# Performance work log

Hardware: AMD Instinct MI355X
Metric: run time of the kernel (lower is better)

Reference implementation:

```python
import jax, jax.numpy as jnp
import numpy as np

B, C, H, W = 32, 256, 56, 56
HEADS, M, EXP = 8, 7, 4


def _rel_pos_index(m):
    # Swin V1 pair-wise relative position index, [m*m, m*m] (static)
    coords = np.stack(np.meshgrid(np.arange(m), np.arange(m), indexing='ij'))  # [2,m,m]
    cf = coords.reshape(2, -1)
    rel = (cf[:, :, None] - cf[:, None, :]).transpose(1, 2, 0).copy()
    rel[:, :, 0] += m - 1
    rel[:, :, 1] += m - 1
    rel[:, :, 0] *= 2 * m - 1
    return jnp.asarray(rel.sum(-1))


def setup_inputs():
    key = jax.random.key(0)
    ks = jax.random.split(key, 8)
    s = lambda k, shp: jax.random.normal(k, shp, jnp.float32) * 0.02
    return {
        'x': jax.random.normal(ks[0], (B, C, H, W), jnp.float32),
        'qkv_w': s(ks[1], (3 * C, C)), 'qkv_b': jnp.zeros((3 * C,), jnp.float32),
        'proj_w': s(ks[2], (C, C)), 'proj_b': jnp.zeros((C,), jnp.float32),
        'bias_table': s(ks[3], ((2 * M - 1) * (2 * M - 1), HEADS)),
        'ln1_g': jnp.ones((C,), jnp.float32), 'ln1_b': jnp.zeros((C,), jnp.float32),
        'ln2_g': jnp.ones((C,), jnp.float32), 'ln2_b': jnp.zeros((C,), jnp.float32),
        'w1': s(ks[4], (EXP * C, C)), 'b1': jnp.zeros((EXP * C,), jnp.float32),
        'w2': s(ks[5], (C, EXP * C)), 'b2': jnp.zeros((C,), jnp.float32),
    }


def _layernorm(x, g, b, eps=1e-5):
    mu = x.mean(-1, keepdims=True)
    var = ((x - mu) ** 2).mean(-1, keepdims=True)
    return (x - mu) * jax.lax.rsqrt(var + eps) * g + b


def _block(x, qkv_w, qkv_b, proj_w, proj_b, bias_table,
           ln1_g, ln1_b, ln2_g, ln2_b, w1, b1, w2, b2):
    Bx, Cx, Hx, Wx = x.shape
    N = M * M
    # window partition: [B,C,H,W] -> [B*nw, M*M, C]
    xp = x.reshape(Bx, Cx, Hx // M, M, Wx // M, M)
    xp = xp.transpose(0, 2, 4, 3, 5, 1).reshape(-1, N, Cx)
    B_ = xp.shape[0]
    # relative self-attention (pre-LN)
    h = _layernorm(xp, ln1_g, ln1_b)
    qkv = (h @ qkv_w.T + qkv_b).reshape(B_, N, 3, HEADS, Cx // HEADS)
    qkv = qkv.transpose(2, 0, 3, 1, 4)  # [3,B_,H,N,d]
    q, k, v = qkv[0], qkv[1], qkv[2]
    q = q * (HEADS ** -0.5)  # note: module scales by num_heads**-0.5 (faithful)
    rel_idx = _rel_pos_index(M)
    bias = bias_table[rel_idx.reshape(-1)].reshape(N, N, HEADS).transpose(2, 0, 1)
    attn = jax.nn.softmax(jnp.einsum('bhnd,bhmd->bhnm', q, k) + bias[None], axis=-1)
    out = jnp.einsum('bhnm,bhmd->bhnd', attn, v).transpose(0, 2, 1, 3).reshape(B_, N, Cx)
    xp = xp + (out @ proj_w.T + proj_b)
    # MLP (1x1 Conv1d == pointwise linear), exact GELU as in torch
    h2 = _layernorm(xp, ln2_g, ln2_b)
    h2 = jax.nn.gelu(h2 @ w1.T + b1, approximate=False)
    xp = xp + (h2 @ w2.T + b2)
    # window reverse: [B*nw, M*M, C] -> [B,C,H,W]
    nwh, nww = Hx // M, Wx // M
    y = xp.reshape(Bx, nwh, nww, M, M, Cx).transpose(0, 5, 1, 3, 2, 4).reshape(Bx, Cx, Hx, Wx)
    return y


def reference(x, qkv_w, qkv_b, proj_w, proj_b, bias_table,
              ln1_g, ln1_b, ln2_g, ln2_b, w1, b1, w2, b2):
    return _block(x, qkv_w, qkv_b, proj_w, proj_b, bias_table,
                  ln1_g, ln1_b, ln2_g, ln2_b, w1, b1, w2, b2)
```

## Files before the change

### kernel.cpp

```cpp
#include <hip/hip_runtime.h>
#include <math.h>

#define TB 256

typedef short bf16x8 __attribute__((ext_vector_type(8)));
typedef short s16x4 __attribute__((ext_vector_type(4)));
typedef float f32x4 __attribute__((ext_vector_type(4)));
typedef unsigned short u16;

__device__ __forceinline__ float b2f(u16 u){
  union{unsigned i; float f;} v; v.i=((unsigned)u)<<16; return v.f;
}
__device__ __forceinline__ u16 f2b(float f){
  union{float ff; unsigned i;} v; v.ff=f;
  return (u16)((v.i + 0x7FFFu + ((v.i>>16)&1u))>>16);
}

__device__ __forceinline__ float gelu(float x){
  float z = fabsf(x)*0.70710678118654752f;
  float t = 1.0f/fmaf(0.3275911f, z, 1.0f);
  float p = t*fmaf(t, fmaf(t, fmaf(t, fmaf(t, 1.061405429f, -1.453152027f), 1.421413741f), -0.284496736f), 0.254829592f);
  float erfz = fmaf(-p, __expf(-z*z), 1.0f);
  float s = (x >= 0.f) ? erfz : -erfz;
  return 0.5f*x*(1.0f + s);
}

__global__ void k_prep(const float* __restrict__ qkv_w, const float* __restrict__ proj_w,
                       const float* __restrict__ w1, const float* __restrict__ w2,
                       const float* __restrict__ btab,
                       u16* __restrict__ wq, u16* __restrict__ wp,
                       u16* __restrict__ w1b, u16* __restrict__ w2b,
                       float* __restrict__ biasT){
  int i = blockIdx.x*TB + threadIdx.x;
  if(i < 196608){ wq[i] = f2b(qkv_w[i]); return; }
  i -= 196608;
  if(i < 65536){ wp[i] = f2b(proj_w[i]); return; }
  i -= 65536;
  if(i < 262144){ w1b[i] = f2b(w1[i]); return; }
  i -= 262144;
  if(i < 262144){ w2b[i] = f2b(w2[i]); return; }
  i -= 262144;
  if(i < 32768){
    int h = i>>12, kq = i&4095, k = kq>>6, q = kq&63;
    float v = 0.f;
    if(k<49 && q<49){
      int qi=q/7, qj=q-qi*7, ki=k/7, kj=k-ki*7;
      v = btab[((qi-ki+6)*13 + (qj-kj+6))*8 + h];
    }
    biasT[i] = v;
  }
}

__global__ __launch_bounds__(256) void k_post(const u16* __restrict__ x2lin, float* __restrict__ out){
  __shared__ u16 tile[12544];
  const int bid = blockIdx.x;
  const int bb = bid>>6, wh=(bid>>3)&7, chunk=bid&7;
  const int wb = bb*64 + wh*8;
  for(int e=threadIdx.x; e<12544; e+=256){
    int ww = e/1568, rem = e - ww*1568, r = rem>>5, cc = rem&31;
    tile[cc*392 + ww*49 + r] = x2lin[(size_t)(wb+ww)*12544 + r*256 + chunk*32 + cc];
  }
  __syncthreads();
  for(int idx=threadIdx.x; idx<12544; idx+=256){
    int c = idx/392, rem = idx - c*392, ii = rem/56, w = rem - ii*56;
    int ww = w/7, j = w - ww*7;
    out[((size_t)(bb*256 + chunk*32 + c))*3136 + (size_t)(wh*7+ii)*56 + w]
        = b2f(tile[c*392 + ww*49 + ii*7 + j]);
  }
}

#define QB_OFF  32768
#define KB_OFF  65536
#define VT_OFF  98304
#define XS_OFF  65536
#define ATT_LDS 131072

__global__ __launch_bounds__(1024,4) void k_attn(
    const float* __restrict__ x,
    const u16* __restrict__ wqkv,  const float* __restrict__ bqkv,
    const u16* __restrict__ wproj, const float* __restrict__ bproj,
    const float* __restrict__ biasT,
    const float* __restrict__ g1, const float* __restrict__ bt1,
    u16* __restrict__ xtbuf)
{
  extern __shared__ char lds[];
  const int tid = threadIdx.x;
  const int wv = tid >> 6, l = tid & 63;
  const int lr = l & 15, lg = l >> 4;
  const unsigned swzA = ((unsigned)(lr & 7)) << 4;
  const unsigned swzR = ((unsigned)((lr>>2) & 3)) << 4;
  const int win = ((blockIdx.x & 7) << 8) | (blockIdx.x >> 3);
  const int bb = win >> 6, wh = (win >> 3) & 7, ww = win & 7;
  const float* xwin = x + (size_t)bb*802816 + (size_t)wh*392 + ww*7;

  float* xs = (float*)(lds + XS_OFF);
  {
    const int j = tid & 7, rbase = tid >> 3;
    #pragma unroll
    for(int it=0; it<14; ++it){
      int run = it*128 + rbase;
      int c = run/7, ii = run - (run/7)*7;
      if(j<7) xs[c*53 + ii*7 + j] = xwin[(size_t)c*3136 + ii*56 + j];
    }
  }
  __syncthreads();

  {
    float gg[4], bgm[4];
    #pragma unroll
    for(int k2=0;k2<4;++k2){ gg[k2]=g1[l+64*k2]; bgm[k2]=bt1[l+64*k2]; }
    #pragma unroll
    for(int s=0;s<4;++s){
      int n = wv + s*16;
      if(n<49){
        float xv[4];
        #pragma unroll
        for(int k2=0;k2<4;++k2) xv[k2] = xs[(l+64*k2)*53 + n];
        float sm=0.f, sq=0.f;
        #pragma unroll
        for(int k2=0;k2<4;++k2){ sm+=xv[k2]; sq+=xv[k2]*xv[k2]; }
        #pragma unroll
        for(int off=32;off>=1;off>>=1){ sm+=__shfl_xor(sm,off); sq+=__shfl_xor(sq,off); }
        float mu=sm*(1.f/256.f), var=sq*(1.f/256.f)-mu*mu;
        float rs=rsqrtf(var+1e-5f);
        #pragma unroll
        for(int k2=0;k2<4;++k2){
          int c=l+64*k2;
          unsigned off2 = (((unsigned)n)*512u + ((unsigned)c)*2u) ^ (((unsigned)(n&7))<<4);
          *(u16*)(lds + off2) = f2b((xv[k2]-mu)*rs*gg[k2]+bgm[k2]);
        }
      }
    }
  }
  for(int m=tid; m<3840; m+=1024) *(u16*)(lds + 49*512 + m*2) = 0;
  __syncthreads();

  for(int m=tid; m<3840; m+=1024){
    int hd = m/480, rm = m - hd*480;
    int d = rm/15, r = 49 + (rm - (rm/15)*15);
    *(u16*)(lds + ((unsigned)(VT_OFF + hd*4096 + d*128 + r*2) ^ ((((unsigned)d)&7u)<<4))) = 0;
  }

  for(int ct=wv; ct<48; ct+=16){
    const u16* wrow = wqkv + ((size_t)(ct*16+lr))*256 + lg*8;
    f32x4 acc[4];
    #pragma unroll
    for(int rt=0;rt<4;++rt) acc[rt]=(f32x4){0.f,0.f,0.f,0.f};
    #pragma unroll
    for(int kq=0; kq<4; ++kq){
      bf16x8 bfr[2];
      #pragma unroll
      for(int k=0;k<2;++k) bfr[k] = *(const bf16x8*)(wrow + kq*64 + k*32);
      #pragma unroll
      for(int rt=0; rt<4; ++rt){
        #pragma unroll
        for(int k=0;k<2;++k){
          bf16x8 afr = *(const bf16x8*)(lds + ((((unsigned)(rt*16+lr))*512u + (unsigned)((kq*2+k)*64+lg*16)) ^ swzA));
          acc[rt] = __builtin_amdgcn_mfma_f32_16x16x32_bf16(bfr[k], afr, acc[rt], 0,0,0);
        }
      }
    }
    f32x4 b4 = *(const f32x4*)(bqkv + ct*16 + lg*4);
    const int s3 = ct>>4, hd = (ct>>1)&7, db = (ct&1)*16 + lg*4;
    #pragma unroll
    for(int rt=0; rt<4; ++rt){
      const int r = rt*16 + lr;
      if(r<49){
        if(s3==0){
          s16x4 pk;
          #pragma unroll
          for(int i=0;i<4;++i) pk[i] = (short)f2b((acc[rt][i]+b4[i])*0.35355339059327373f);
          *(s16x4*)(lds + ((unsigned)(QB_OFF + hd*4096 + r*64 + db*2) ^ swzR)) = pk;
        } else if(s3==1){
          s16x4 pk;
          #pragma unroll
          for(int i=0;i<4;++i) pk[i] = (short)f2b(acc[rt][i]+b4[i]);
          *(s16x4*)(lds + ((unsigned)(KB_OFF + hd*4096 + r*64 + db*2) ^ swzR)) = pk;
        } else {
          #pragma unroll
          for(int i=0;i<4;++i)
            *(u16*)(lds + ((unsigned)(VT_OFF + hd*4096 + (db+i)*128 + r*2) ^ ((((unsigned)(db+i))&7u)<<4))) = f2b(acc[rt][i]+b4[i]);
        }
      }
    }
  }
  __syncthreads();

  {
    const int h = wv & 7, half = wv >> 3;
    s16x4 pkk[2][4];
    #pragma unroll
    for(int j=0;j<2;++j){
      const int qt = half*2 + j;
      bf16x8 qf = *(const bf16x8*)(lds + ((unsigned)(QB_OFF + h*4096 + (qt*16+lr)*64 + lg*16) ^ swzR));
      f32x4 st[4];
      #pragma unroll
      for(int kt=0;kt<4;++kt){
        bf16x8 kfk = *(const bf16x8*)(lds + ((unsigned)(KB_OFF + h*4096 + (kt*16+lr)*64 + lg*16) ^ swzR));
        f32x4 bini;
        #pragma unroll
        for(int i=0;i<4;++i) bini[i] = biasT[h*4096 + (kt*16+lg*4+i)*64 + qt*16+lr];
        st[kt] = __builtin_amdgcn_mfma_f32_16x16x32_bf16(kfk, qf, bini, 0,0,0);
      }
      #pragma unroll
      for(int i=0;i<4;++i)
        if(!(lg==0 && i==0)) st[3][i] = -1e30f;

      float mx = -1e30f;
      #pragma unroll
      for(int kt=0;kt<4;++kt)
        #pragma unroll
        for(int i=0;i<4;++i) mx = fmaxf(mx, st[kt][i]);
      mx = fmaxf(mx, __shfl_xor(mx,16));
      mx = fmaxf(mx, __shfl_xor(mx,32));
      float su = 0.f;
      #pragma unroll
      for(int kt=0;kt<4;++kt)
        #pragma unroll
        for(int i=0;i<4;++i){ float p = __expf(st[kt][i]-mx); st[kt][i]=p; su+=p; }
      su += __shfl_xor(su,16);
      su += __shfl_xor(su,32);
      float inv = 1.f/su;
      #pragma unroll
      for(int kt=0;kt<4;++kt)
        #pragma unroll
        for(int i=0;i<4;++i) pkk[j][kt][i] = (short)f2b(st[kt][i]*inv);
    }
    __syncthreads();

    char* Pb = lds + h*8192;
    #pragma unroll
    for(int j=0;j<2;++j){
      const unsigned rq = (unsigned)((half*2+j)*16 + lr);
      #pragma unroll
      for(int kt=0;kt<4;++kt)
        *(s16x4*)(Pb + ((rq*128u + (unsigned)(kt*32+lg*8)) ^ swzA)) = pkk[j][kt];
    }
    #pragma unroll
    for(int j=0;j<2;++j){
      const int qt = half*2 + j;
      const unsigned rq = (unsigned)(qt*16 + lr);
      bf16x8 pf0 = *(const bf16x8*)(Pb + ((rq*128u + (unsigned)(lg*16)) ^ swzA));
      bf16x8 pf1 = *(const bf16x8*)(Pb + ((rq*128u + (unsigned)(64+lg*16)) ^ swzA));
      #pragma unroll
      for(int dt=0;dt<2;++dt){
        bf16x8 vf0 = *(const bf16x8*)(lds + ((unsigned)(VT_OFF + h*4096 + (dt*16+lr)*128 + lg*16) ^ swzA));
        bf16x8 vf1 = *(const bf16x8*)(lds + ((unsigned)(VT_OFF + h*4096 + (dt*16+lr)*128 + 64+lg*16) ^ swzA));
        f32x4 o = {0.f,0.f,0.f,0.f};
        o = __builtin_amdgcn_mfma_f32_16x16x32_bf16(pf0, vf0, o, 0,0,0);
        o = __builtin_amdgcn_mfma_f32_16x16x32_bf16(pf1, vf1, o, 0,0,0);
        #pragma unroll
        for(int i=0;i<4;++i)
          *(u16*)(lds + ((unsigned)(KB_OFF + h*4096 + (qt*16+lg*4+i)*64 + (dt*16+lr)*2) ^ (((unsigned)lg)<<4))) = f2b(o[i]);
      }
    }
  }
  __syncthreads();

  {
    const int c = wv*16 + lr;
    const u16* wrow = wproj + (size_t)c*256 + lg*8;
    const float pbP = bproj[c];
    f32x4 acc[4];
    #pragma unroll
    for(int mt=0;mt<4;++mt) acc[mt]=(f32x4){0.f,0.f,0.f,0.f};
    #pragma unroll
    for(int kq=0; kq<4; ++kq){
      bf16x8 bfrP[2];
      #pragma unroll
      for(int k=0;k<2;++k) bfrP[k] = *(const bf16x8*)(wrow + kq*64 + k*32);
      #pragma unroll
      for(int mt=0; mt<4; ++mt){
        #pragma unroll
        for(int k=0;k<2;++k){
          bf16x8 afr = *(const bf16x8*)(lds + ((unsigned)(KB_OFF + (kq*2+k)*4096 + (mt*16+lr)*64 + lg*16) ^ swzR));
          acc[mt] = __builtin_amdgcn_mfma_f32_16x16x32_bf16(afr, bfrP[k], acc[mt], 0,0,0);
        }
      }
    }
    #pragma unroll
    for(int mt=0; mt<4; ++mt){
      #pragma unroll
      for(int i=0;i<4;++i){
        int r = mt*16 + lg*4 + i;
        if(r<49){
          int ii=r/7, jj=r-ii*7;
          float val = acc[mt][i] + pbP + xwin[(size_t)c*3136 + ii*56 + jj];
          *(u16*)(lds + ((((unsigned)r)*512u + ((unsigned)c)*2u) ^ (((unsigned)(r&7))<<4))) = f2b(val);
        }
      }
    }
  }
  __syncthreads();

  for(int u=tid; u<12544; u+=1024){
    int r = u>>8, c = u&255;
    xtbuf[(size_t)win*12544 + u] = *(const u16*)(lds + ((((unsigned)r)*512u + ((unsigned)c)*2u) ^ (((unsigned)(r&7))<<4)));
  }
}

#define MLP_LDS 98304

__global__ __launch_bounds__(1024,4) void k_mlp(
    const u16* __restrict__ xtbuf,
    const u16* __restrict__ w1, const float* __restrict__ b1v,
    const u16* __restrict__ w2, const float* __restrict__ b2v,
    const float* __restrict__ g2, const float* __restrict__ bt2,
    u16* __restrict__ x2lin)
{
  extern __shared__ char lds[];
  const int tid = threadIdx.x;
  const int wv = tid >> 6, l = tid & 63;
  const int lr = l & 15, lg = l >> 4;
  const unsigned swzA = ((unsigned)(lr & 7)) << 4;
  const int win = ((blockIdx.x & 7) << 8) | (blockIdx.x >> 3);
  const size_t base = (size_t)win*12544;

  {
    float gg[4], bb2[4];
    #pragma unroll
    for(int k2=0;k2<4;++k2){ gg[k2]=g2[l+64*k2]; bb2[k2]=bt2[l+64*k2]; }
    #pragma unroll
    for(int rr=0; rr<4; ++rr){
      int r = wv*4 + rr;
      if(r<49){
        float v[4];
        #pragma unroll
        for(int k2=0;k2<4;++k2) v[k2] = b2f(xtbuf[base + r*256 + l + 64*k2]);
        float sm=v[0]+v[1]+v[2]+v[3];
        float sq=v[0]*v[0]+v[1]*v[1]+v[2]*v[2]+v[3]*v[3];
        #pragma unroll
        for(int off=32;off>=1;off>>=1){ sm+=__shfl_xor(sm,off); sq+=__shfl_xor(sq,off); }
        float mu=sm*(1.f/256.f), var=sq*(1.f/256.f)-mu*mu, rs=rsqrtf(var+1e-5f);
        #pragma unroll
        for(int k2=0;k2<4;++k2){
          int c=l+64*k2;
          unsigned off2 = (((unsigned)r)*512u + ((unsigned)c)*2u) ^ (((unsigned)(r&7))<<4);
          *(u16*)(lds + off2) = f2b((v[k2]-mu)*rs*gg[k2]+bb2[k2]);
        }
      }
    }
  }
  for(int m=tid; m<3840; m+=1024){
    int r = 49 + (m>>8), c = m & 255;
    *(u16*)(lds + ((((unsigned)r)*512u + ((unsigned)c)*2u) ^ (((unsigned)(r&7))<<4))) = 0;
  }
  __syncthreads();

  const int hcol = wv*16 + lr;
  f32x4 acc2[4];
  #pragma unroll
  for(int mt=0;mt<4;++mt) acc2[mt]=(f32x4){0.f,0.f,0.f,0.f};

  {
    const u16* wrow = w1 + (size_t)hcol*256 + lg*8;
    const float bias1 = b1v[hcol];
    f32x4 acc[4];
    #pragma unroll
    for(int mt=0;mt<4;++mt) acc[mt]=(f32x4){0.f,0.f,0.f,0.f};
    #pragma unroll
    for(int kq=0; kq<4; ++kq){
      bf16x8 bfr1[2];
      #pragma unroll
      for(int k=0;k<2;++k) bfr1[k] = *(const bf16x8*)(wrow + kq*64 + k*32);
      #pragma unroll
      for(int mt=0; mt<4; ++mt){
        #pragma unroll
        for(int k=0;k<2;++k){
          bf16x8 afr = *(const bf16x8*)(lds + ((((unsigned)(mt*16+lr))*512u + (unsigned)((kq*2+k)*64+lg*16)) ^ swzA));
          acc[mt] = __builtin_amdgcn_mfma_f32_16x16x32_bf16(afr, bfr1[k], acc[mt], 0,0,0);
        }
      }
    }
    #pragma unroll
    for(int mt=0; mt<4; ++mt)
      #pragma unroll
      for(int i2=0;i2<4;++i2){
        int r = mt*16 + lg*4 + i2;
        *(u16*)(lds + 32768u + ((((unsigned)r)*512u + ((unsigned)hcol)*2u) ^ (((unsigned)(r&7))<<4))) = f2b(gelu(acc[mt][i2]+bias1));
      }
  }
  __syncthreads();

  for(int kc=0; kc<4; ++kc){
    if(kc<3){
      const int gcol = (kc+1)*256 + hcol;
      const u16* wrow = w1 + (size_t)gcol*256 + lg*8;
      const float biasN = b1v[gcol];
      const unsigned dst = ((kc+1)&1) ? 65536u : 32768u;
      f32x4 acc[4];
      #pragma unroll
      for(int mt=0;mt<4;++mt) acc[mt]=(f32x4){0.f,0.f,0.f,0.f};
      #pragma unroll
      for(int kq=0; kq<4; ++kq){
        bf16x8 bfrN[2];
        #pragma unroll
        for(int k=0;k<2;++k) bfrN[k] = *(const bf16x8*)(wrow + kq*64 + k*32);
        #pragma unroll
        for(int mt=0; mt<4; ++mt){
          #pragma unroll
          for(int k=0;k<2;++k){
            bf16x8 afr = *(const bf16x8*)(lds + ((((unsigned)(mt*16+lr))*512u + (unsigned)((kq*2+k)*64+lg*16)) ^ swzA));
            acc[mt] = __builtin_amdgcn_mfma_f32_16x16x32_bf16(afr, bfrN[k], acc[mt], 0,0,0);
          }
        }
      }
      #pragma unroll
      for(int mt=0; mt<4; ++mt)
        #pragma unroll
        for(int i2=0;i2<4;++i2){
          int r = mt*16 + lg*4 + i2;
          *(u16*)(lds + dst + ((((unsigned)r)*512u + ((unsigned)hcol)*2u) ^ (((unsigned)(r&7))<<4))) = f2b(gelu(acc[mt][i2]+biasN));
        }
    }
    {
      const u16* wrow = w2 + (size_t)hcol*1024 + kc*256 + lg*8;
      const unsigned src = (kc&1) ? 65536u : 32768u;
      __builtin_amdgcn_s_setprio(1);
      #pragma unroll
      for(int kq=0; kq<4; ++kq){
        bf16x8 bfr2[2];
        #pragma unroll
        for(int k=0;k<2;++k) bfr2[k] = *(const bf16x8*)(wrow + kq*64 + k*32);
        #pragma unroll
        for(int mt=0; mt<4; ++mt){
          #pragma unroll
          for(int k=0;k<2;++k){
            bf16x8 afr = *(const bf16x8*)(lds + src + ((((unsigned)(mt*16+lr))*512u + (unsigned)((kq*2+k)*64+lg*16)) ^ swzA));
            acc2[mt] = __builtin_amdgcn_mfma_f32_16x16x32_bf16(afr, bfr2[k], acc2[mt], 0,0,0);
          }
        }
      }
      __builtin_amdgcn_s_setprio(0);
    }
    __syncthreads();
  }

  u16* fin = (u16*)(lds + 32768);
  {
    const int c = hcol;
    const float biasc = b2v[c];
    #pragma unroll
    for(int mt=0; mt<4; ++mt){
      #pragma unroll
      for(int i2=0;i2<4;++i2){
        int r = mt*16 + lg*4 + i2;
        if(r<49){
          float resid = b2f(xtbuf[base + r*256 + c]);
          fin[r*256 + c] = f2b(acc2[mt][i2] + biasc + resid);
        }
      }
    }
  }
  __syncthreads();

  for(int u=tid; u<12544; u+=1024)
    x2lin[base + u] = fin[u];
}

extern "C" void kernel_launch(void* const* d_in, const int* in_sizes, int n_in,
                              void* d_out, int out_size, void* d_ws, size_t ws_size,
                              hipStream_t stream) {
  const float* x      = (const float*)d_in[0];
  const float* qkv_w  = (const float*)d_in[1];
  const float* qkv_b  = (const float*)d_in[2];
  const float* proj_w = (const float*)d_in[3];
  const float* proj_b = (const float*)d_in[4];
  const float* btab   = (const float*)d_in[5];
  const float* ln1g   = (const float*)d_in[6];
  const float* ln1b   = (const float*)d_in[7];
  const float* ln2g   = (const float*)d_in[8];
  const float* ln2b   = (const float*)d_in[9];
  const float* w1     = (const float*)d_in[10];
  const float* b1     = (const float*)d_in[11];
  const float* w2     = (const float*)d_in[12];
  const float* b2     = (const float*)d_in[13];

  char* ws = (char*)d_ws;
  float* biasT = (float*)ws;
  u16*   wq    = (u16*)(ws + 131072);
  u16*   wp    = (u16*)(ws + 524288);
  u16*   w1b   = (u16*)(ws + 655360);
  u16*   w2b   = (u16*)(ws + 1179648);
  u16*   x2l   = (u16*)(ws + 1703936);
  u16*   xtb   = (u16*)d_out;

  k_prep<<<3200, TB, 0, stream>>>(qkv_w, proj_w, w1, w2, btab, wq, wp, w1b, w2b, biasT);

  hipFuncSetAttribute((const void*)k_attn, hipFuncAttributeMaxDynamicSharedMemorySize, ATT_LDS);
  hipFuncSetAttribute((const void*)k_mlp,  hipFuncAttributeMaxDynamicSharedMemorySize, MLP_LDS);
  k_attn<<<2048, 1024, ATT_LDS, stream>>>(x, wq, qkv_b, wp, proj_b, biasT, ln1g, ln1b, xtb);
  k_mlp <<<2048, 1024, MLP_LDS, stream>>>(xtb, w1b, b1, w2b, b2, ln2g, ln2b, x2l);
  k_post<<<2048, 256, 0, stream>>>(x2l, (float*)d_out);
}
```

Measured before the change: 714.6 us.

## Retile MLP kernel over 128 contiguous token rows to remove window padding

The MLP kernel now processes 128 consecutive token rows per block (784 blocks of 512 threads) instead of one 49-token window padded to 64 rows. This removes the wasted MFMA work on padding rows and doubles the number of rows that reuse each weight fragment loaded from global memory. Each wave now covers 32 output columns with twice as many row tiles. In exchange, the GELU intermediate is no longer double-buffered, so each chunk gains an extra barrier and loses the overlap between the first and second GEMM. LDS per block grows to 128KB with fewer waves per block, which may reduce latency hiding.

After: 882.3 us. 1.23x slower.

```diff
diff --git a/kernel.cpp b/kernel.cpp
--- a/kernel.cpp
+++ b/kernel.cpp
@@ -299,9 +299,9 @@
   }
 }
 
-#define MLP_LDS 98304
-
-__global__ __launch_bounds__(1024,4) void k_mlp(
+#define MLP_LDS 131072
+
+__global__ __launch_bounds__(512,2) void k_mlp(
     const u16* __restrict__ xtbuf,
     const u16* __restrict__ w1, const float* __restrict__ b1v,
     const u16* __restrict__ w2, const float* __restrict__ b2v,
@@ -313,149 +313,115 @@
   const int wv = tid >> 6, l = tid & 63;
   const int lr = l & 15, lg = l >> 4;
   const unsigned swzA = ((unsigned)(lr & 7)) << 4;
-  const int win = ((blockIdx.x & 7) << 8) | (blockIdx.x >> 3);
-  const size_t base = (size_t)win*12544;
+  const size_t rbase = (size_t)blockIdx.x * 128;
 
   {
     float gg[4], bb2[4];
     #pragma unroll
     for(int k2=0;k2<4;++k2){ gg[k2]=g2[l+64*k2]; bb2[k2]=bt2[l+64*k2]; }
     #pragma unroll
-    for(int rr=0; rr<4; ++rr){
-      int r = wv*4 + rr;
-      if(r<49){
-        float v[4];
-        #pragma unroll
-        for(int k2=0;k2<4;++k2) v[k2] = b2f(xtbuf[base + r*256 + l + 64*k2]);
-        float sm=v[0]+v[1]+v[2]+v[3];
-        float sq=v[0]*v[0]+v[1]*v[1]+v[2]*v[2]+v[3]*v[3];
-        #pragma unroll
-        for(int off=32;off>=1;off>>=1){ sm+=__shfl_xor(sm,off); sq+=__shfl_xor(sq,off); }
-        float mu=sm*(1.f/256.f), var=sq*(1.f/256.f)-mu*mu, rs=rsqrtf(var+1e-5f);
-        #pragma unroll
-        for(int k2=0;k2<4;++k2){
-          int c=l+64*k2;
-          unsigned off2 = (((unsigned)r)*512u + ((unsigned)c)*2u) ^ (((unsigned)(r&7))<<4);
-          *(u16*)(lds + off2) = f2b((v[k2]-mu)*rs*gg[k2]+bb2[k2]);
-        }
-      }
-    }
-  }
-  for(int m=tid; m<3840; m+=1024){
-    int r = 49 + (m>>8), c = m & 255;
-    *(u16*)(lds + ((((unsigned)r)*512u + ((unsigned)c)*2u) ^ (((unsigned)(r&7))<<4))) = 0;
-  }
-  __syncthreads();
-
-  const int hcol = wv*16 + lr;
-  f32x4 acc2[4];
+    for(int rr=0; rr<16; ++rr){
+      int r = wv*16 + rr;
+      float v[4];
+      #pragma unroll
+      for(int k2=0;k2<4;++k2) v[k2] = b2f(xtbuf[(rbase + r)*256 + l + 64*k2]);
+      float sm=v[0]+v[1]+v[2]+v[3];
+      float sq=v[0]*v[0]+v[1]*v[1]+v[2]*v[2]+v[3]*v[3];
+      #pragma unroll
+      for(int off=32;off>=1;off>>=1){ sm+=__shfl_xor(sm,off); sq+=__shfl_xor(sq,off); }
+      float mu=sm*(1.f/256.f), var=sq*(1.f/256.f)-mu*mu, rs=rsqrtf(var+1e-5f);
+      #pragma unroll
+      for(int k2=0;k2<4;++k2){
+        int c=l+64*k2;
+        unsigned off2 = (((unsigned)r)*512u + ((unsigned)c)*2u) ^ (((unsigned)(r&7))<<4);
+        *(u16*)(lds + off2) = f2b((v[k2]-mu)*rs*gg[k2]+bb2[k2]);
+      }
+    }
+  }
+  __syncthreads();
+
+  f32x4 acc2[2][8];
   #pragma unroll
-  for(int mt=0;mt<4;++mt) acc2[mt]=(f32x4){0.f,0.f,0.f,0.f};
-
-  {
-    const u16* wrow = w1 + (size_t)hcol*256 + lg*8;
-    const float bias1 = b1v[hcol];
-    f32x4 acc[4];
-    #pragma unroll
-    for(int mt=0;mt<4;++mt) acc[mt]=(f32x4){0.f,0.f,0.f,0.f};
-    #pragma unroll
-    for(int kq=0; kq<4; ++kq){
-      bf16x8 bfr1[2];
-      #pragma unroll
-      for(int k=0;k<2;++k) bfr1[k] = *(const bf16x8*)(wrow + kq*64 + k*32);
-      #pragma unroll
-      for(int mt=0; mt<4; ++mt){
-        #pragma unroll
-        for(int k=0;k<2;++k){
-          bf16x8 afr = *(const bf16x8*)(lds + ((((unsigned)(mt*16+lr))*512u + (unsigned)((kq*2+k)*64+lg*16)) ^ swzA));
-          acc[mt] = __builtin_amdgcn_mfma_f32_16x16x32_bf16(afr, bfr1[k], acc[mt], 0,0,0);
-        }
-      }
-    }
-    #pragma unroll
-    for(int mt=0; mt<4; ++mt)
-      #pragma unroll
-      for(int i2=0;i2<4;++i2){
-        int r = mt*16 + lg*4 + i2;
-        *(u16*)(lds + 32768u + ((((unsigned)r)*512u + ((unsigned)hcol)*2u) ^ (((unsigned)(r&7))<<4))) = f2b(gelu(acc[mt][i2]+bias1));
-      }
-  }
-  __syncthreads();
+  for(int nt=0;nt<2;++nt)
+    #pragma unroll
+    for(int mt=0;mt<8;++mt) acc2[nt][mt]=(f32x4){0.f,0.f,0.f,0.f};
 
   for(int kc=0; kc<4; ++kc){
-    if(kc<3){
-      const int gcol = (kc+1)*256 + hcol;
+    #pragma unroll
+    for(int nt=0; nt<2; ++nt){
+      const int hcol = wv*32 + nt*16 + lr;
+      const int gcol = kc*256 + hcol;
       const u16* wrow = w1 + (size_t)gcol*256 + lg*8;
-      const float biasN = b1v[gcol];
-      const unsigned dst = ((kc+1)&1) ? 65536u : 32768u;
-      f32x4 acc[4];
-      #pragma unroll
-      for(int mt=0;mt<4;++mt) acc[mt]=(f32x4){0.f,0.f,0.f,0.f};
+      const float bias1 = b1v[gcol];
+      f32x4 acc[8];
+      #pragma unroll
+      for(int mt=0;mt<8;++mt) acc[mt]=(f32x4){0.f,0.f,0.f,0.f};
       #pragma unroll
       for(int kq=0; kq<4; ++kq){
-        bf16x8 bfrN[2];
-        #pragma unroll
-        for(int k=0;k<2;++k) bfrN[k] = *(const bf16x8*)(wrow + kq*64 + k*32);
-        #pragma unroll
-        for(int mt=0; mt<4; ++mt){
+        bf16x8 bfr[2];
+        #pragma unroll
+        for(int k=0;k<2;++k) bfr[k] = *(const bf16x8*)(wrow + kq*64 + k*32);
+        #pragma unroll
+        for(int mt=0; mt<8; ++mt){
           #pragma unroll
           for(int k=0;k<2;++k){
             bf16x8 afr = *(const bf16x8*)(lds + ((((unsigned)(mt*16+lr))*512u + (unsigned)((kq*2+k)*64+lg*16)) ^ swzA));
-            acc[mt] = __builtin_amdgcn_mfma_f32_16x16x32_bf16(afr, bfrN[k], acc[mt], 0,0,0);
+            acc[mt] = __builtin_amdgcn_mfma_f32_16x16x32_bf16(afr, bfr[k], acc[mt], 0,0,0);
           }
         }
       }
       #pragma unroll
-      for(int mt=0; mt<4; ++mt)
+      for(int mt=0; mt<8; ++mt)
         #pragma unroll
         for(int i2=0;i2<4;++i2){
           int r = mt*16 + lg*4 + i2;
-          *(u16*)(lds + dst + ((((unsigned)r)*512u + ((unsigned)hcol)*2u) ^ (((unsigned)(r&7))<<4))) = f2b(gelu(acc[mt][i2]+biasN));
-        }
-    }
-    {
-      const u16* wrow = w2 + (size_t)hcol*1024 + kc*256 + lg*8;
-      const unsigned src = (kc&1) ? 65536u : 32768u;
-      __builtin_amdgcn_s_setprio(1);
+          *(u16*)(lds + 65536u + ((((unsigned)r)*512u + ((unsigned)hcol)*2u) ^ (((unsigned)(r&7))<<4))) = f2b(gelu(acc[mt][i2]+bias1));
+        }
+    }
+    __syncthreads();
+    __builtin_amdgcn_s_setprio(1);
+    #pragma unroll
+    for(int nt=0; nt<2; ++nt){
+      const int c = wv*32 + nt*16 + lr;
+      const u16* wrow = w2 + (size_t)c*1024 + kc*256 + lg*8;
       #pragma unroll
       for(int kq=0; kq<4; ++kq){
         bf16x8 bfr2[2];
         #pragma unroll
         for(int k=0;k<2;++k) bfr2[k] = *(const bf16x8*)(wrow + kq*64 + k*32);
         #pragma unroll
-        for(int mt=0; mt<4; ++mt){
+        for(int mt=0; mt<8; ++mt){
           #pragma unroll
           for(int k=0;k<2;++k){
-            bf16x8 afr = *(const bf16x8*)(lds + src + ((((unsigned)(mt*16+lr))*512u + (unsigned)((kq*2+k)*64+lg*16)) ^ swzA));
-            acc2[mt] = __builtin_amdgcn_mfma_f32_16x16x32_bf16(afr, bfr2[k], acc2[mt], 0,0,0);
+            bf16x8 afr = *(const bf16x8*)(lds + 65536u + ((((unsigned)(mt*16+lr))*512u + (unsigned)((kq*2+k)*64+lg*16)) ^ swzA));
+            acc2[nt][mt] = __builtin_amdgcn_mfma_f32_16x16x32_bf16(afr, bfr2[k], acc2[nt][mt], 0,0,0);
           }
         }
       }
-      __builtin_amdgcn_s_setprio(0);
-    }
+    }
+    __builtin_amdgcn_s_setprio(0);
     __syncthreads();
   }
 
-  u16* fin = (u16*)(lds + 32768);
-  {
-    const int c = hcol;
+  u16* fin = (u16*)(lds + 65536);
+  #pragma unroll
+  for(int nt=0; nt<2; ++nt){
+    const int c = wv*32 + nt*16 + lr;
     const float biasc = b2v[c];
     #pragma unroll
-    for(int mt=0; mt<4; ++mt){
+    for(int mt=0; mt<8; ++mt){
       #pragma unroll
       for(int i2=0;i2<4;++i2){
         int r = mt*16 + lg*4 + i2;
-        if(r<49){
-          float resid = b2f(xtbuf[base + r*256 + c]);
-          fin[r*256 + c] = f2b(acc2[mt][i2] + biasc + resid);
-        }
-      }
-    }
-  }
-  __syncthreads();
-
-  for(int u=tid; u<12544; u+=1024)
-    x2lin[base + u] = fin[u];
+        float resid = b2f(xtbuf[(rbase + r)*256 + c]);
+        fin[r*256 + c] = f2b(acc2[nt][mt][i2] + biasc + resid);
+      }
+    }
+  }
+  __syncthreads();
+
+  for(int u=tid; u<32768; u+=512)
+    x2lin[rbase*256 + u] = fin[u];
 }
 
 extern "C" void kernel_launch(void* const* d_in, const int* in_sizes, int n_in,
@@ -490,6 +456,6 @@
   hipFuncSetAttribute((const void*)k_attn, hipFuncAttributeMaxDynamicSharedMemorySize, ATT_LDS);
   hipFuncSetAttribute((const void*)k_mlp,  hipFuncAttributeMaxDynamicSharedMemorySize, MLP_LDS);
   k_attn<<<2048, 1024, ATT_LDS, stream>>>(x, wq, qkv_b, wp, proj_b, biasT, ln1g, ln1b, xtb);
-  k_mlp <<<2048, 1024, MLP_LDS, stream>>>(xtb, w1b, b1, w2b, b2, ln2g, ln2b, x2l);
+  k_mlp <<<784, 512, MLP_LDS, stream>>>(xtb, w1b, b1, w2b, b2, ln2g, ln2b, x2l);
   k_post<<<2048, 256, 0, stream>>>(x2l, (float*)d_out);
 }
```
